# Kernel tuning notes

Measured on AMD Instinct MI355X. Metric: run time of the kernel, lower is better.

The kernel has to match this reference:

```python
import jax, jax.numpy as jnp
import numpy as np
import math

B, S, D, H = 2, 2048, 1024, 16
DK = D // H


def setup_inputs() -> dict:
    key = jax.random.key(0)
    ks = jax.random.split(key, 5)
    scale = 0.02
    x = jax.random.normal(ks[0], (B, S, D), dtype=jnp.float32)
    wq = jax.random.normal(ks[1], (D, D), dtype=jnp.float32) * scale
    wk = jax.random.normal(ks[2], (D, D), dtype=jnp.float32) * scale
    wv = jax.random.normal(ks[3], (D, D), dtype=jnp.float32) * scale
    wo = jax.random.normal(ks[4], (D, D), dtype=jnp.float32) * scale
    bq = jnp.zeros((D,), jnp.float32)
    bk = jnp.zeros((D,), jnp.float32)
    bv = jnp.zeros((D,), jnp.float32)
    bo = jnp.zeros((D,), jnp.float32)
    # causal mask: mask==0 positions are filled with -inf in the original
    mask = jnp.tril(jnp.ones((S, S), dtype=bool))[None, None]  # [1,1,S,S]
    return {"x": x, "mask": mask, "wq": wq, "bq": bq, "wk": wk, "bk": bk,
            "wv": wv, "bv": bv, "wo": wo, "bo": bo}


def reference(x, mask, wq, bq, wk, bk, wv, bv, wo, bo):
    b, sl, d = x.shape
    # torch Linear: y = x @ W^T + b
    def proj(w, bias):
        y = jnp.einsum('bsd,ed->bse', x, w) + bias
        return y.reshape(b, sl, H, DK).transpose(0, 2, 1, 3)  # [B,H,S,DK]
    q = proj(wq, bq)
    k = proj(wk, bk)
    v = proj(wv, bv)
    sc = jnp.einsum('bhqd,bhkd->bhqk', q, k) / math.sqrt(DK)  # [B,H,S,S]
    sc = jnp.where(mask, sc, -jnp.inf)
    aw = jax.nn.softmax(sc, axis=-1)
    # dropout is identity in eval mode (reference baseline)
    ao = jnp.einsum('bhqk,bhkd->bhqd', aw, v)
    ao = ao.transpose(0, 2, 1, 3).reshape(b, sl, d)
    out = jnp.einsum('bsd,ed->bse', ao, wo) + bo
    return out
```

## Files before the change

### kernel.cpp

```cpp
#include <hip/hip_runtime.h>
#include <cstdint>
#include <cstddef>

#define Bb 2
#define Ss 2048
#define Dd 1024
#define Hh 16
#define DKk 64

typedef unsigned short ushort_t;
typedef __bf16 bf16x8 __attribute__((ext_vector_type(8)));
typedef float f32x4 __attribute__((ext_vector_type(4)));
typedef unsigned short us8 __attribute__((ext_vector_type(8)));
typedef unsigned short us4 __attribute__((ext_vector_type(4)));

__device__ __forceinline__ ushort_t f2bf(float f) {
  __bf16 h = (__bf16)f;
  return __builtin_bit_cast(unsigned short, h);
}

__device__ __forceinline__ void gload_lds16(const void* g, void* l) {
  __builtin_amdgcn_global_load_lds(
      (__attribute__((address_space(1))) void*)(g),
      (__attribute__((address_space(3))) void*)(l),
      16, 0, 0);
}

__global__ __launch_bounds__(256) void cast_all(
    const float* __restrict__ x, const float* __restrict__ w0,
    const float* __restrict__ w1, const float* __restrict__ w2,
    const float* __restrict__ w3, ushort_t* __restrict__ dx,
    ushort_t* __restrict__ dw) {
  const int b = blockIdx.x;
  const float* s;
  ushort_t* d;
  int i;
  if (b < 2048) {
    s = x; d = dx; i = b * 256 + threadIdx.x;
  } else {
    const int w = (b - 2048) >> 9;
    s = (w == 0) ? w0 : (w == 1) ? w1 : (w == 2) ? w2 : w3;
    d = dw + (size_t)w * 1048576;
    i = ((b - 2048) & 511) * 256 + threadIdx.x;
  }
  const float4* sp = (const float4*)s;
  float4 a = sp[2 * i], c = sp[2 * i + 1];
  us8 o;
  o[0] = f2bf(a.x); o[1] = f2bf(a.y); o[2] = f2bf(a.z); o[3] = f2bf(a.w);
  o[4] = f2bf(c.x); o[5] = f2bf(c.y); o[6] = f2bf(c.z); o[7] = f2bf(c.w);
  ((us8*)d)[i] = o;
}

__global__ __launch_bounds__(256) void gemm0_k(
    const ushort_t* __restrict__ A, const ushort_t* __restrict__ W,
    const float* __restrict__ b0, const float* __restrict__ b1,
    const float* __restrict__ b2,
    ushort_t* __restrict__ oQ, ushort_t* __restrict__ oK,
    ushort_t* __restrict__ oVT) {
  constexpr int Kd = 1024;
  __shared__ ushort_t As[128 * 32];
  __shared__ ushort_t Bs[128 * 32];
  const int tid = threadIdx.x;
  const int lane = tid & 63;
  const int wave = tid >> 6;
  const int m0 = blockIdx.y * 128;
  const int n0 = blockIdx.x * 128;
  const int lr = lane & 15;
  const int lg = lane >> 4;
  const int srow = lane >> 2;
  const int scol = (lane & 3) * 8;
  const int ar = (wave >> 1) * 64;
  const int bc = (wave & 1) * 64;

  f32x4 acc[4][4] = {};

  for (int kt = 0; kt < Kd / 32; ++kt) {
    const int k0 = kt * 32;
#pragma unroll
    for (int c = 0; c < 2; ++c) {
      const int seg = wave * 2 + c;
      const int row = seg * 16 + srow;
      gload_lds16(A + (size_t)(m0 + row) * Kd + k0 + scol, (char*)As + seg * 1024);
      gload_lds16(W + (size_t)(n0 + row) * Kd + k0 + scol, (char*)Bs + seg * 1024);
    }
    __syncthreads();
    bf16x8 af[4], bfr[4];
#pragma unroll
    for (int i = 0; i < 4; ++i)
      af[i] = *(const bf16x8*)&As[(ar + i * 16 + lr) * 32 + lg * 8];
#pragma unroll
    for (int j = 0; j < 4; ++j)
      bfr[j] = *(const bf16x8*)&Bs[(bc + j * 16 + lr) * 32 + lg * 8];
#pragma unroll
    for (int i = 0; i < 4; ++i)
#pragma unroll
      for (int j = 0; j < 4; ++j)
        acc[i][j] = __builtin_amdgcn_mfma_f32_16x16x32_bf16(af[i], bfr[j],
                                                            acc[i][j], 0, 0, 0);
    __syncthreads();
  }

#pragma unroll
  for (int i = 0; i < 4; ++i) {
    const int mrow = m0 + ar + i * 16 + lg * 4;
#pragma unroll
    for (int j = 0; j < 4; ++j) {
      const int n = n0 + bc + j * 16 + lr;
      const int sel = n >> 10;
      const int nn = n & 1023;
      const float bias = (sel == 0 ? b0 : sel == 1 ? b1 : b2)[nn];
      const int h = nn >> 6, dk = nn & 63;
      const int bidx = mrow >> 11;
      const int s = mrow & 2047;
      const int bh = bidx * Hh + h;
      if (sel == 2) {
        us4 pk;
#pragma unroll
        for (int r = 0; r < 4; ++r) pk[r] = f2bf(acc[i][j][r] + bias);
        *(us4*)&oVT[((size_t)bh * DKk + dk) * Ss + s] = pk;
      } else {
        ushort_t* dst = (sel == 0) ? oQ : oK;
        const float mul = (sel == 0) ? 0.1803368842f : 1.0f;
#pragma unroll
        for (int r = 0; r < 4; ++r)
          dst[((size_t)bh * Ss + (s + r)) * DKk + dk] =
              f2bf((acc[i][j][r] + bias) * mul);
      }
    }
  }
}

__global__ __launch_bounds__(256) void gemm1_k(const ushort_t* __restrict__ A,
                                               const ushort_t* __restrict__ W,
                                               const float* __restrict__ b0,
                                               float* __restrict__ oF) {
  constexpr int Kd = 1024;
  __shared__ ushort_t As[128 * 32];
  __shared__ ushort_t Bs[64 * 32];
  const int tid = threadIdx.x;
  const int lane = tid & 63;
  const int wave = tid >> 6;
  const int m0 = blockIdx.y * 128;
  const int n0 = blockIdx.x * 64;
  const int lr = lane & 15;
  const int lg = lane >> 4;
  const int srow = lane >> 2;
  const int scol = (lane & 3) * 8;

  f32x4 acc[2][4] = {};

  for (int kt = 0; kt < Kd / 32; ++kt) {
    const int k0 = kt * 32;
#pragma unroll
    for (int c = 0; c < 2; ++c) {
      const int seg = wave * 2 + c;
      const int row = seg * 16 + srow;
      gload_lds16(A + (size_t)(m0 + row) * Kd + k0 + scol, (char*)As + seg * 1024);
    }
    {
      const int row = wave * 16 + srow;
      gload_lds16(W + (size_t)(n0 + row) * Kd + k0 + scol, (char*)Bs + wave * 1024);
    }
    __syncthreads();
    bf16x8 af[2], bfr[4];
#pragma unroll
    for (int i = 0; i < 2; ++i)
      af[i] = *(const bf16x8*)&As[(wave * 32 + i * 16 + lr) * 32 + lg * 8];
#pragma unroll
    for (int j = 0; j < 4; ++j)
      bfr[j] = *(const bf16x8*)&Bs[(j * 16 + lr) * 32 + lg * 8];
#pragma unroll
    for (int i = 0; i < 2; ++i)
#pragma unroll
      for (int j = 0; j < 4; ++j)
        acc[i][j] = __builtin_amdgcn_mfma_f32_16x16x32_bf16(af[i], bfr[j],
                                                            acc[i][j], 0, 0, 0);
    __syncthreads();
  }

#pragma unroll
  for (int i = 0; i < 2; ++i) {
    const int mrow = m0 + wave * 32 + i * 16 + lg * 4;
#pragma unroll
    for (int j = 0; j < 4; ++j) {
      const int n = n0 + j * 16 + lr;
      const float bias = b0[n];
#pragma unroll
      for (int r = 0; r < 4; ++r)
        oF[(size_t)(mrow + r) * Dd + n] = acc[i][j][r] + bias;
    }
  }
}

__global__ __launch_bounds__(256, 4) void attn_k(const ushort_t* __restrict__ Qg,
                                                 const ushort_t* __restrict__ Kg,
                                                 const ushort_t* __restrict__ Vt,
                                                 ushort_t* __restrict__ AO) {
  __shared__ ushort_t Ks[2][64 * 64];
  __shared__ ushort_t Pl[4][16 * 72];
  const int tid = threadIdx.x, lane = tid & 63, wave = tid >> 6;
  const int bx = blockIdx.x;
  const int bh = bx & 31;
  const int r_ = bx >> 8;
  const int sub = (bx >> 5) & 7;
  const int g = (3 - r_) * 8 + ((r_ & 1) ? 7 - sub : sub);
  const int lr = lane & 15, lg = lane >> 4;
  const ushort_t* Qp = Qg + (size_t)bh * Ss * DKk;
  const ushort_t* Kp = Kg + (size_t)bh * Ss * DKk;
  const ushort_t* Vp = Vt + (size_t)bh * DKk * Ss;
  ushort_t* P = Pl[wave];
  const int s_row = lane >> 3;
  const int s_slot = (lane & 7) ^ s_row;
  const int sw = lr & 7;
  const int q0 = g * 64 + wave * 16;
  const int nt = g + 1;

  auto stageK = [&](int t, int buf) {
    const int rb = wave * 16;
#pragma unroll
    for (int c = 0; c < 2; ++c)
      gload_lds16(Kp + (size_t)(t * 64 + rb + c * 8 + s_row) * DKk + s_slot * 8,
                  &Ks[buf][(rb + c * 8) * 64]);
  };

  stageK(0, 0);

  bf16x8 qf[2];
#pragma unroll
  for (int ks = 0; ks < 2; ++ks)
    qf[ks] = *(const bf16x8*)&Qp[(size_t)(q0 + lr) * DKk + ks * 32 + lg * 8];

  bf16x8 onesv;
#pragma unroll
  for (int e = 0; e < 8; ++e) onesv[e] = (__bf16)1.0f;

  f32x4 o[4] = {};
  f32x4 l4 = {};
  float m_ = -3e38f;

  __syncthreads();

  for (int t = 0; t < nt; ++t) {
    const int cb = t & 1;
    if (t + 1 < nt) stageK(t + 1, cb ^ 1);
    const int j0 = t * 64;
    const bool diag = (t == nt - 1);
    const int nct = diag ? wave + 1 : 4;

    bf16x8 vt[4][2];
#pragma unroll
    for (int dj = 0; dj < 4; ++dj)
#pragma unroll
      for (int ksp = 0; ksp < 2; ++ksp)
        vt[dj][ksp] = *(const bf16x8*)&Vp[(size_t)(dj * 16 + lr) * Ss + j0 +
                                          ksp * 32 + lg * 8];

    f32x4 sc[4];
#pragma unroll
    for (int ct = 0; ct < 4; ++ct) {
      if (ct < nct) {
        const int krow = ct * 16 + lr;
        const bf16x8 k0v = *(const bf16x8*)&Ks[cb][krow * 64 + ((lg ^ sw) * 8)];
        const bf16x8 k1v =
            *(const bf16x8*)&Ks[cb][krow * 64 + (((4 | lg) ^ sw) * 8)];
        f32x4 z = {};
        z = __builtin_amdgcn_mfma_f32_16x16x32_bf16(k0v, qf[0], z, 0, 0, 0);
        z = __builtin_amdgcn_mfma_f32_16x16x32_bf16(k1v, qf[1], z, 0, 0, 0);
        sc[ct] = z;
      }
    }
    if (diag) {
#pragma unroll
      for (int ct = 0; ct < 4; ++ct)
        if (ct == nct - 1)
#pragma unroll
          for (int r = 0; r < 4; ++r)
            if (lg * 4 + r > lr) sc[ct][r] = -1e30f;
    }

    float mx = -3e38f;
#pragma unroll
    for (int ct = 0; ct < 4; ++ct)
      if (ct < nct)
#pragma unroll
        for (int r = 0; r < 4; ++r) mx = fmaxf(mx, sc[ct][r]);
    mx = fmaxf(mx, __shfl_xor(mx, 16, 64));
    mx = fmaxf(mx, __shfl_xor(mx, 32, 64));
    const float mnew = fmaxf(m_, mx);
    const float fs = __builtin_exp2f(m_ - mnew);
    m_ = mnew;
#pragma unroll
    for (int ct = 0; ct < 4; ++ct) {
      if (ct < nct) {
        float p0 = __builtin_exp2f(sc[ct][0] - m_);
        float p1 = __builtin_exp2f(sc[ct][1] - m_);
        float p2 = __builtin_exp2f(sc[ct][2] - m_);
        float p3 = __builtin_exp2f(sc[ct][3] - m_);
        us4 pk;
        pk[0] = f2bf(p0); pk[1] = f2bf(p1); pk[2] = f2bf(p2); pk[3] = f2bf(p3);
        *(us4*)&P[lr * 72 + ct * 16 + lg * 4] = pk;
      } else {
        us4 zz = {};
        *(us4*)&P[lr * 72 + ct * 16 + lg * 4] = zz;
      }
    }

#pragma unroll
    for (int dj = 0; dj < 4; ++dj)
#pragma unroll
      for (int r = 0; r < 4; ++r) o[dj][r] *= fs;
    l4[0] *= fs;

    asm volatile("s_waitcnt lgkmcnt(0)" ::: "memory");
    bf16x8 pa[2];
#pragma unroll
    for (int ksp = 0; ksp < 2; ++ksp)
      pa[ksp] = *(const bf16x8*)&P[lr * 72 + ksp * 32 + lg * 8];

#pragma unroll
    for (int ksp = 0; ksp < 2; ++ksp)
      l4 = __builtin_amdgcn_mfma_f32_16x16x32_bf16(onesv, pa[ksp], l4, 0, 0, 0);
#pragma unroll
    for (int dj = 0; dj < 4; ++dj)
#pragma unroll
      for (int ksp = 0; ksp < 2; ++ksp)
        o[dj] = __builtin_amdgcn_mfma_f32_16x16x32_bf16(vt[dj][ksp], pa[ksp],
                                                        o[dj], 0, 0, 0);

    __syncthreads();
  }

  const int bb = bh >> 4, hh = bh & 15;
  const float inv = 1.0f / l4[0];
#pragma unroll
  for (int dj = 0; dj < 4; ++dj) {
    us4 pk;
#pragma unroll
    for (int r = 0; r < 4; ++r) pk[r] = f2bf(o[dj][r] * inv);
    *(us4*)&AO[((size_t)bb * Ss + q0 + lr) * Dd + hh * 64 + dj * 16 + lg * 4] =
        pk;
  }
}

extern "C" void kernel_launch(void* const* d_in, const int* in_sizes, int n_in,
                              void* d_out, int out_size, void* d_ws, size_t ws_size,
                              hipStream_t stream) {
  const float* x  = (const float*)d_in[0];
  const float* wq = (const float*)d_in[2];
  const float* bq = (const float*)d_in[3];
  const float* wk = (const float*)d_in[4];
  const float* bk = (const float*)d_in[5];
  const float* wv = (const float*)d_in[6];
  const float* bv = (const float*)d_in[7];
  const float* wo = (const float*)d_in[8];
  const float* bo = (const float*)d_in[9];

  ushort_t* ws   = (ushort_t*)d_ws;
  ushort_t* xb   = ws;
  ushort_t* wqkv = xb + 4096 * 1024;
  ushort_t* wob  = wqkv + 3072 * 1024;
  ushort_t* Qb   = wob + 1024 * 1024;
  ushort_t* Kb   = Qb + 4194304;
  ushort_t* VTb  = Kb + 4194304;
  ushort_t* AOb  = xb;

  cast_all<<<4096, 256, 0, stream>>>(x, wq, wk, wv, wo, xb, wqkv);

  gemm0_k<<<dim3(24, 32), 256, 0, stream>>>(xb, wqkv, bq, bk, bv, Qb, Kb, VTb);
  attn_k<<<1024, 256, 0, stream>>>(Qb, Kb, VTb, AOb);
  gemm1_k<<<dim3(16, 32), 256, 0, stream>>>(AOb, wob, bo, (float*)d_out);
}
```

Before: 141.0 us.

## Keep softmax probabilities in registers by permuting the K index of the PV MFMA

Removes the per-wave LDS round-trip for the P tile (store, lgkmcnt wait, reload) by building the PV MFMA operand directly from the score accumulator registers. To match the permuted K ordering, V columns are now loaded as two 4-element chunks per operand instead of one 8-element load. This frees LDS and removes a wait, but doubles the number of narrower global loads for V.

```diff
diff --git a/kernel.cpp b/kernel.cpp
--- a/kernel.cpp
+++ b/kernel.cpp
@@ -10,6 +10,7 @@
 
 typedef unsigned short ushort_t;
 typedef __bf16 bf16x8 __attribute__((ext_vector_type(8)));
+typedef __bf16 bf16x4 __attribute__((ext_vector_type(4)));
 typedef float f32x4 __attribute__((ext_vector_type(4)));
 typedef unsigned short us8 __attribute__((ext_vector_type(8)));
 typedef unsigned short us4 __attribute__((ext_vector_type(4)));
@@ -197,7 +198,6 @@
                                                  const ushort_t* __restrict__ Vt,
                                                  ushort_t* __restrict__ AO) {
   __shared__ ushort_t Ks[2][64 * 64];
-  __shared__ ushort_t Pl[4][16 * 72];
   const int tid = threadIdx.x, lane = tid & 63, wave = tid >> 6;
   const int bx = blockIdx.x;
   const int bh = bx & 31;
@@ -208,7 +208,6 @@
   const ushort_t* Qp = Qg + (size_t)bh * Ss * DKk;
   const ushort_t* Kp = Kg + (size_t)bh * Ss * DKk;
   const ushort_t* Vp = Vt + (size_t)bh * DKk * Ss;
-  ushort_t* P = Pl[wave];
   const int s_row = lane >> 3;
   const int s_slot = (lane & 7) ^ s_row;
   const int sw = lr & 7;
@@ -251,9 +250,16 @@
 #pragma unroll
     for (int dj = 0; dj < 4; ++dj)
 #pragma unroll
-      for (int ksp = 0; ksp < 2; ++ksp)
-        vt[dj][ksp] = *(const bf16x8*)&Vp[(size_t)(dj * 16 + lr) * Ss + j0 +
-                                          ksp * 32 + lg * 8];
+      for (int c = 0; c < 2; ++c) {
+        const bf16x4 va =
+            *(const bf16x4*)&Vp[(size_t)(dj * 16 + lr) * Ss + j0 + c * 32 + lg * 4];
+        const bf16x4 vb = *(const bf16x4*)&Vp[(size_t)(dj * 16 + lr) * Ss + j0 +
+                                              c * 32 + 16 + lg * 4];
+        bf16x8 v;
+        v[0] = va[0]; v[1] = va[1]; v[2] = va[2]; v[3] = va[3];
+        v[4] = vb[0]; v[5] = vb[1]; v[6] = vb[2]; v[7] = vb[3];
+        vt[dj][c] = v;
+      }
 
     f32x4 sc[4];
 #pragma unroll
@@ -289,19 +295,19 @@
     const float mnew = fmaxf(m_, mx);
     const float fs = __builtin_exp2f(m_ - mnew);
     m_ = mnew;
+    bf16x4 pb[4];
 #pragma unroll
     for (int ct = 0; ct < 4; ++ct) {
       if (ct < nct) {
-        float p0 = __builtin_exp2f(sc[ct][0] - m_);
-        float p1 = __builtin_exp2f(sc[ct][1] - m_);
-        float p2 = __builtin_exp2f(sc[ct][2] - m_);
-        float p3 = __builtin_exp2f(sc[ct][3] - m_);
-        us4 pk;
-        pk[0] = f2bf(p0); pk[1] = f2bf(p1); pk[2] = f2bf(p2); pk[3] = f2bf(p3);
-        *(us4*)&P[lr * 72 + ct * 16 + lg * 4] = pk;
+        bf16x4 pbv;
+        pbv[0] = (__bf16)__builtin_exp2f(sc[ct][0] - m_);
+        pbv[1] = (__bf16)__builtin_exp2f(sc[ct][1] - m_);
+        pbv[2] = (__bf16)__builtin_exp2f(sc[ct][2] - m_);
+        pbv[3] = (__bf16)__builtin_exp2f(sc[ct][3] - m_);
+        pb[ct] = pbv;
       } else {
-        us4 zz = {};
-        *(us4*)&P[lr * 72 + ct * 16 + lg * 4] = zz;
+        bf16x4 zz = {};
+        pb[ct] = zz;
       }
     }
 
@@ -311,20 +317,25 @@
       for (int r = 0; r < 4; ++r) o[dj][r] *= fs;
     l4[0] *= fs;
 
-    asm volatile("s_waitcnt lgkmcnt(0)" ::: "memory");
     bf16x8 pa[2];
 #pragma unroll
-    for (int ksp = 0; ksp < 2; ++ksp)
-      pa[ksp] = *(const bf16x8*)&P[lr * 72 + ksp * 32 + lg * 8];
-
-#pragma unroll
-    for (int ksp = 0; ksp < 2; ++ksp)
-      l4 = __builtin_amdgcn_mfma_f32_16x16x32_bf16(onesv, pa[ksp], l4, 0, 0, 0);
+    for (int c = 0; c < 2; ++c) {
+      bf16x8 v;
+      v[0] = pb[2 * c][0]; v[1] = pb[2 * c][1];
+      v[2] = pb[2 * c][2]; v[3] = pb[2 * c][3];
+      v[4] = pb[2 * c + 1][0]; v[5] = pb[2 * c + 1][1];
+      v[6] = pb[2 * c + 1][2]; v[7] = pb[2 * c + 1][3];
+      pa[c] = v;
+    }
+
+#pragma unroll
+    for (int c = 0; c < 2; ++c)
+      l4 = __builtin_amdgcn_mfma_f32_16x16x32_bf16(onesv, pa[c], l4, 0, 0, 0);
 #pragma unroll
     for (int dj = 0; dj < 4; ++dj)
 #pragma unroll
-      for (int ksp = 0; ksp < 2; ++ksp)
-        o[dj] = __builtin_amdgcn_mfma_f32_16x16x32_bf16(vt[dj][ksp], pa[ksp],
+      for (int c = 0; c < 2; ++c)
+        o[dj] = __builtin_amdgcn_mfma_f32_16x16x32_bf16(vt[dj][c], pa[c],
                                                         o[dj], 0, 0, 0);
 
     __syncthreads();
```

New measurement: 198.3 us. +40.6%, slower.

## Split attention KV range in two halves and merge with a combine kernel

Applied to the files above, without the earlier changes.

The attention kernel now divides each query tile's causal key range into two halves, launching twice as many blocks. Each block writes a partial normalized output plus a log-sum-exp value, and a new combine kernel merges the two partials into the final layout. The aim is better load balance and occupancy for causal attention, where long rows otherwise dominate. The cost is an extra kernel launch, extra global traffic for the bf16 partials, and an extra rounding step when the halves are merged.

```diff
diff --git a/kernel.cpp b/kernel.cpp
--- a/kernel.cpp
+++ b/kernel.cpp
@@ -17,6 +17,10 @@
 __device__ __forceinline__ ushort_t f2bf(float f) {
   __bf16 h = (__bf16)f;
   return __builtin_bit_cast(unsigned short, h);
+}
+__device__ __forceinline__ float bf2f(ushort_t u) {
+  unsigned x = ((unsigned)u) << 16;
+  return __builtin_bit_cast(float, x);
 }
 
 __device__ __forceinline__ void gload_lds16(const void* g, void* l) {
@@ -195,16 +199,32 @@
 __global__ __launch_bounds__(256, 4) void attn_k(const ushort_t* __restrict__ Qg,
                                                  const ushort_t* __restrict__ Kg,
                                                  const ushort_t* __restrict__ Vt,
-                                                 ushort_t* __restrict__ AO) {
+                                                 ushort_t* __restrict__ Ob,
+                                                 float* __restrict__ Ml) {
   __shared__ ushort_t Ks[2][64 * 64];
   __shared__ ushort_t Pl[4][16 * 72];
   const int tid = threadIdx.x, lane = tid & 63, wave = tid >> 6;
   const int bx = blockIdx.x;
-  const int bh = bx & 31;
-  const int r_ = bx >> 8;
-  const int sub = (bx >> 5) & 7;
-  const int g = (3 - r_) * 8 + ((r_ & 1) ? 7 - sub : sub);
+  const int g = 31 - (bx >> 6);
+  const int bh = (bx >> 1) & 31;
+  const int half = bx & 1;
   const int lr = lane & 15, lg = lane >> 4;
+  const int q0 = g * 64 + wave * 16;
+  const int ntt = g + 1;
+  const int h0 = (ntt + 1) >> 1;
+  const int t0 = half ? h0 : 0;
+  const int t1 = half ? ntt : h0;
+  const size_t prow = (size_t)(half * 65536 + bh * 2048 + q0 + lr);
+
+  if (t0 >= t1) {
+    us4 zz = {};
+#pragma unroll
+    for (int dj = 0; dj < 4; ++dj)
+      *(us4*)&Ob[prow * 64 + dj * 16 + lg * 4] = zz;
+    if (lg == 0) Ml[prow] = -3e38f;
+    return;
+  }
+
   const ushort_t* Qp = Qg + (size_t)bh * Ss * DKk;
   const ushort_t* Kp = Kg + (size_t)bh * Ss * DKk;
   const ushort_t* Vp = Vt + (size_t)bh * DKk * Ss;
@@ -212,8 +232,6 @@
   const int s_row = lane >> 3;
   const int s_slot = (lane & 7) ^ s_row;
   const int sw = lr & 7;
-  const int q0 = g * 64 + wave * 16;
-  const int nt = g + 1;
 
   auto stageK = [&](int t, int buf) {
     const int rb = wave * 16;
@@ -223,7 +241,7 @@
                   &Ks[buf][(rb + c * 8) * 64]);
   };
 
-  stageK(0, 0);
+  stageK(t0, 0);
 
   bf16x8 qf[2];
 #pragma unroll
@@ -240,11 +258,11 @@
 
   __syncthreads();
 
-  for (int t = 0; t < nt; ++t) {
-    const int cb = t & 1;
-    if (t + 1 < nt) stageK(t + 1, cb ^ 1);
+  for (int t = t0; t < t1; ++t) {
+    const int cb = (t - t0) & 1;
+    if (t + 1 < t1) stageK(t + 1, cb ^ 1);
     const int j0 = t * 64;
-    const bool diag = (t == nt - 1);
+    const bool diag = (t == g);
     const int nct = diag ? wave + 1 : 4;
 
     bf16x8 vt[4][2];
@@ -330,15 +348,40 @@
     __syncthreads();
   }
 
-  const int bb = bh >> 4, hh = bh & 15;
   const float inv = 1.0f / l4[0];
 #pragma unroll
   for (int dj = 0; dj < 4; ++dj) {
     us4 pk;
 #pragma unroll
     for (int r = 0; r < 4; ++r) pk[r] = f2bf(o[dj][r] * inv);
-    *(us4*)&AO[((size_t)bb * Ss + q0 + lr) * Dd + hh * 64 + dj * 16 + lg * 4] =
-        pk;
+    *(us4*)&Ob[prow * 64 + dj * 16 + lg * 4] = pk;
+  }
+  if (lg == 0) Ml[prow] = m_ + __builtin_log2f(l4[0]);
+}
+
+__global__ __launch_bounds__(256) void comb_k(const ushort_t* __restrict__ Ob,
+                                              const float* __restrict__ Ml,
+                                              ushort_t* __restrict__ AO) {
+  const int R = blockIdx.x * 256 + threadIdx.x;
+  const float L1 = Ml[R], L2 = Ml[65536 + R];
+  const float M = fmaxf(L1, L2);
+  float w1 = __builtin_exp2f(L1 - M);
+  float w2 = __builtin_exp2f(L2 - M);
+  const float inv = 1.0f / (w1 + w2);
+  w1 *= inv; w2 *= inv;
+  const us8* p1 = (const us8*)&Ob[(size_t)R * 64];
+  const us8* p2 = (const us8*)&Ob[(size_t)(65536 + R) * 64];
+  const int bh = R >> 11, s = R & 2047;
+  const int bb = bh >> 4, hh = bh & 15;
+  ushort_t* dst = &AO[((size_t)bb * Ss + s) * Dd + hh * 64];
+#pragma unroll
+  for (int c = 0; c < 8; ++c) {
+    const us8 a = p1[c], b = p2[c];
+    us8 o;
+#pragma unroll
+    for (int e = 0; e < 8; ++e)
+      o[e] = f2bf(bf2f(a[e]) * w1 + bf2f(b[e]) * w2);
+    ((us8*)dst)[c] = o;
   }
 }
 
@@ -362,11 +405,14 @@
   ushort_t* Qb   = wob + 1024 * 1024;
   ushort_t* Kb   = Qb + 4194304;
   ushort_t* VTb  = Kb + 4194304;
+  ushort_t* Obp  = VTb + 4194304;
+  float*    Mlp  = (float*)(Obp + 8388608);
   ushort_t* AOb  = xb;
 
   cast_all<<<4096, 256, 0, stream>>>(x, wq, wk, wv, wo, xb, wqkv);
 
   gemm0_k<<<dim3(24, 32), 256, 0, stream>>>(xb, wqkv, bq, bk, bv, Qb, Kb, VTb);
-  attn_k<<<1024, 256, 0, stream>>>(Qb, Kb, VTb, AOb);
+  attn_k<<<2048, 256, 0, stream>>>(Qb, Kb, VTb, Obp, Mlp);
+  comb_k<<<256, 256, 0, stream>>>(Obp, Mlp, AOb);
   gemm1_k<<<dim3(16, 32), 256, 0, stream>>>(AOb, wob, bo, (float*)d_out);
 }
```

Result: slower. 154.7 us (+9.7%).
